# Kernel optimization log

Hardware: AMD Instinct MI355X
Metric: run time of the kernel (lower is better)

## Reference

```python
import jax, jax.numpy as jnp
import numpy as np

B, S, D, H = 4, 2048, 1024, 16
HD = D // H


def setup_inputs() -> dict:
    key = jax.random.key(0)
    ks = jax.random.split(key, 12)
    scale = 1.0 / np.sqrt(D)
    inp = {
        "query": jax.random.normal(ks[0], (B, S, D), jnp.float32),
        "key": jax.random.normal(ks[1], (B, S, D), jnp.float32),
        "value": jax.random.normal(ks[2], (B, S, D), jnp.float32),
        "mask": jax.random.randint(ks[3], (B, 1, S, S), 0, 2).astype(jnp.float32),
        "Wq": jax.random.normal(ks[4], (D, D), jnp.float32) * scale,
        "bq": jnp.zeros((D,), jnp.float32),
        "Wk": jax.random.normal(ks[5], (D, D), jnp.float32) * scale,
        "bk": jnp.zeros((D,), jnp.float32),
        "Wv": jax.random.normal(ks[6], (D, D), jnp.float32) * scale,
        "bv": jnp.zeros((D,), jnp.float32),
        "Wo": jax.random.normal(ks[7], (D, D), jnp.float32) * scale,
        "bo": jnp.zeros((D,), jnp.float32),
    }
    return inp


def reference(query, key, value, mask, Wq, bq, Wk, bk, Wv, bv, Wo, bo):
    # projections, then split heads: [B, S, D] -> [B, H, S, HD]
    def split_heads(x):
        return x.reshape(B, S, H, HD).transpose(0, 2, 1, 3)

    q = split_heads(query @ Wq + bq)
    k = split_heads(key @ Wk + bk)
    v = split_heads(value @ Wv + bv)

    # scores [B, H, Sq, Sk]
    logits = jnp.einsum("bhqd,bhkd->bhqk", q, k) / jnp.sqrt(jnp.float32(HD))
    logits = logits + mask * (-1e9)
    attn = jax.nn.softmax(logits, axis=-1)
    out = jnp.einsum("bhqk,bhkd->bhqd", attn, v)  # [B, H, Sq, HD]
    out = out.transpose(0, 2, 1, 3).reshape(B, S, D)
    return out @ Wo + bo
```

## Files before the change

kernel.cpp:

```cpp
#include <hip/hip_runtime.h>

#define DI __device__ __forceinline__

typedef __attribute__((ext_vector_type(8))) short short8v;
typedef __attribute__((ext_vector_type(4))) float f32x4;

static constexpr int B_ = 4, S_ = 2048, D_ = 1024, H_ = 16, HD_ = 64;
static constexpr int M_ = B_ * S_;

DI unsigned short f2bf(float f) {
  unsigned u = __builtin_bit_cast(unsigned, f);
  u = (u + 0x7fffu + ((u >> 16) & 1u)) >> 16;
  return (unsigned short)u;
}

DI unsigned cvt_pk_bf16(float lo, float hi) {
  unsigned r;
  asm("v_cvt_pk_bf16_f32 %0, %1, %2" : "=v"(r) : "v"(lo), "v"(hi));
  return r;
}

DI void async_copy16(const void* g, void* l) {
  __builtin_amdgcn_global_load_lds((const __attribute__((address_space(1))) void*)g,
                                   (__attribute__((address_space(3))) void*)l, 16, 0, 0);
}

__global__ __launch_bounds__(256) void cast_bf16_kernel(const float* __restrict__ in,
                                                        unsigned short* __restrict__ out,
                                                        int n4) {
  int i = blockIdx.x * blockDim.x + threadIdx.x;
  int stride = gridDim.x * blockDim.x;
  for (; i < n4; i += stride) {
    float4 v = reinterpret_cast<const float4*>(in)[i];
    ushort4 o;
    o.x = f2bf(v.x); o.y = f2bf(v.y); o.z = f2bf(v.z); o.w = f2bf(v.w);
    reinterpret_cast<ushort4*>(out)[i] = o;
  }
}

__global__ __launch_bounds__(256) void transpose_cast_kernel(const float* __restrict__ W,
                                                             unsigned short* __restrict__ Wt,
                                                             int n) {
  __shared__ float t[32][33];
  int bx = blockIdx.x * 32, by = blockIdx.y * 32;
  int x = threadIdx.x, y0 = threadIdx.y;
#pragma unroll
  for (int yy = 0; yy < 32; yy += 8)
    t[y0 + yy][x] = W[(long)(by + y0 + yy) * n + bx + x];
  __syncthreads();
#pragma unroll
  for (int yy = 0; yy < 32; yy += 8)
    Wt[(long)(bx + y0 + yy) * n + by + x] = f2bf(t[x][y0 + yy]);
}

__global__ __launch_bounds__(256) void pack_mask_kernel(const float* __restrict__ mask,
                                                        unsigned long long* __restrict__ bits,
                                                        int nwords) {
  int lane = threadIdx.x & 63;
  int wpb = blockDim.x >> 6;
  int w = blockIdx.x * wpb + (threadIdx.x >> 6);
  int stride = gridDim.x * wpb;
  for (; w < nwords; w += stride) {
    float v = mask[(long)w * 64 + lane];
    unsigned long long b = __ballot(v > 0.5f);
    if (lane == 0) {
      int bb = w >> 16, q = (w >> 5) & 2047, kt64 = w & 31;
      bits[((long)bb << 16) | (kt64 << 11) | q] = b;
    }
  }
}

template <int MODE>
__global__ __launch_bounds__(256) void gemm_bt_kernel(const unsigned short* __restrict__ A,
                                                      const unsigned short* __restrict__ Bt,
                                                      const float* __restrict__ bias,
                                                      void* __restrict__ out,
                                                      int Mdim, int Ndim, int Kdim, float scale) {
  __shared__ unsigned short As[128 * 32];
  __shared__ unsigned short Bs[128 * 32];
  const int tid = threadIdx.x;
  const int lane = tid & 63;
  const int w = tid >> 6;
  const int g = lane >> 4;
  const int l15 = lane & 15;
  const int bm = blockIdx.x * 128;
  const int bn = blockIdx.y * 128;
  const int wr = w >> 1, wc = w & 1;

  f32x4 zero = {0.f, 0.f, 0.f, 0.f};
  f32x4 acc[4][4];
#pragma unroll
  for (int i = 0; i < 4; ++i)
#pragma unroll
    for (int j = 0; j < 4; ++j) acc[i][j] = zero;

  const int srow = lane >> 2;
  const int scol = (lane & 3) * 8;

  for (int k0 = 0; k0 < Kdim; k0 += 32) {
#pragma unroll
    for (int i = 0; i < 2; ++i) {
      int q = w * 2 + i;
      int row = q * 16 + srow;
      async_copy16(&A[(long)(bm + row) * Kdim + k0 + scol], &As[q * 512]);
      async_copy16(&Bt[(long)(bn + row) * Kdim + k0 + scol], &Bs[q * 512]);
    }
    __syncthreads();
    short8v a[4], b[4];
#pragma unroll
    for (int i = 0; i < 4; ++i)
      a[i] = *reinterpret_cast<const short8v*>(&As[(wr * 64 + i * 16 + l15) * 32 + g * 8]);
#pragma unroll
    for (int j = 0; j < 4; ++j)
      b[j] = *reinterpret_cast<const short8v*>(&Bs[(wc * 64 + j * 16 + l15) * 32 + g * 8]);
#pragma unroll
    for (int i = 0; i < 4; ++i)
#pragma unroll
      for (int j = 0; j < 4; ++j)
        acc[i][j] = __builtin_amdgcn_mfma_f32_16x16x32_bf16(a[i], b[j], acc[i][j], 0, 0, 0);
    __syncthreads();
  }

#pragma unroll
  for (int jj = 0; jj < 4; ++jj) {
    int n = bn + wc * 64 + jj * 16 + l15;
    float bs = bias[n];
#pragma unroll
    for (int i = 0; i < 4; ++i) {
      int m0 = bm + wr * 64 + i * 16 + g * 4;
      if (MODE == 0) {
        unsigned short* o = (unsigned short*)out;
#pragma unroll
        for (int r = 0; r < 4; ++r)
          o[(long)(m0 + r) * Ndim + n] = f2bf((acc[i][jj][r] + bs) * scale);
      } else if (MODE == 1) {
        int b2 = m0 >> 11, s0 = m0 & 2047;
        int s0p = (s0 & ~31) | (((s0 >> 2) & 3) << 3) | (((s0 >> 4) & 1) << 2);
        int h2 = n >> 6, d2 = n & 63;
        unsigned short* o = (unsigned short*)out;
        ushort4 v;
        v.x = f2bf(acc[i][jj][0] + bs);
        v.y = f2bf(acc[i][jj][1] + bs);
        v.z = f2bf(acc[i][jj][2] + bs);
        v.w = f2bf(acc[i][jj][3] + bs);
        *reinterpret_cast<ushort4*>(&o[((long)((b2 * 16 + h2) * 64 + d2) << 11) + s0p]) = v;
      } else {
        float* o = (float*)out;
#pragma unroll
        for (int r = 0; r < 4; ++r)
          o[(long)(m0 + r) * Ndim + n] = acc[i][jj][r] + bs;
      }
    }
  }
}

__global__ __launch_bounds__(256, 3) void attn_kernel(const unsigned short* __restrict__ Q,
                                                      const unsigned short* __restrict__ Kb,
                                                      const unsigned short* __restrict__ Vt,
                                                      const unsigned long long* __restrict__ mbits,
                                                      unsigned short* __restrict__ attn) {
  __shared__ unsigned short Ks[64 * 64];
  __shared__ unsigned short Vs[64 * 64];
  const int lane = threadIdx.x & 63;
  const int w = threadIdx.x >> 6;
  const int g = lane >> 4;
  const int l15 = lane & 15;
  const int qt = blockIdx.x;
  const int bh = blockIdx.y;
  const int b = bh >> 4, h = bh & 15;
  const int q0 = qt * 128 + w * 32 + l15;

  const unsigned short* qp = Q + ((long)b * S_ + q0) * D_ + h * HD_ + g * 8;
  short8v qfr[2][2];
  qfr[0][0] = *reinterpret_cast<const short8v*>(qp);
  qfr[0][1] = *reinterpret_cast<const short8v*>(qp + 32);
  qfr[1][0] = *reinterpret_cast<const short8v*>(qp + 16 * D_);
  qfr[1][1] = *reinterpret_cast<const short8v*>(qp + 16 * D_ + 32);

  const int srow = lane >> 3;
  const int schunk = ((lane & 7) ^ (lane >> 3)) * 8;
  const unsigned short* kstage = Kb + (long)b * S_ * D_ + h * HD_;
  const unsigned short* vstage = Vt + (long)bh * HD_ * S_;

  f32x4 zero = {0.f, 0.f, 0.f, 0.f};
  f32x4 oacc[2][4];
#pragma unroll
  for (int qf = 0; qf < 2; ++qf)
#pragma unroll
    for (int d = 0; d < 4; ++d) oacc[qf][d] = zero;
  float m_run[2] = {-1e30f, -1e30f}, l_run[2] = {0.f, 0.f};

  const unsigned long long* mbase = mbits + ((long)b << 16);
  const int swz = l15 & 7;

  for (int kt = 0; kt < S_; kt += 64) {
    unsigned long long mw0 = mbase[((kt >> 6) << 11) + q0];
    unsigned long long mw1 = mbase[((kt >> 6) << 11) + q0 + 16];
#pragma unroll
    for (int i = 0; i < 2; ++i) {
      int blk8 = w * 2 + i;
      async_copy16(&kstage[(long)(kt + blk8 * 8 + srow) * D_ + schunk], &Ks[blk8 * 512]);
      async_copy16(&vstage[(long)(blk8 * 8 + srow) * S_ + kt + schunk], &Vs[blk8 * 512]);
    }
    __syncthreads();

    f32x4 lt[2][4];
#pragma unroll
    for (int g2 = 0; g2 < 4; ++g2) {
      const unsigned short* kr = &Ks[(g2 * 16 + l15) * 64];
      short8v kf0 = *reinterpret_cast<const short8v*>(&kr[(g ^ swz) * 8]);
      short8v kf1 = *reinterpret_cast<const short8v*>(&kr[((g + 4) ^ swz) * 8]);
#pragma unroll
      for (int qf = 0; qf < 2; ++qf) {
        f32x4 c = zero;
        c = __builtin_amdgcn_mfma_f32_16x16x32_bf16(kf0, qfr[qf][0], c, 0, 0, 0);
        c = __builtin_amdgcn_mfma_f32_16x16x32_bf16(kf1, qfr[qf][1], c, 0, 0, 0);
        lt[qf][g2] = c;
      }
    }

    short8v pfr[2][2];
#pragma unroll
    for (int qf = 0; qf < 2; ++qf) {
      unsigned long long mw = qf ? mw1 : mw0;
      float tmax = -1e30f;
#pragma unroll
      for (int g2 = 0; g2 < 4; ++g2)
#pragma unroll
        for (int r = 0; r < 4; ++r) {
          int krel = g2 * 16 + g * 4 + r;
          float v = ((mw >> krel) & 1ull) ? -1e30f : lt[qf][g2][r];
          lt[qf][g2][r] = v;
          tmax = fmaxf(tmax, v);
        }
      tmax = fmaxf(tmax, __shfl_xor(tmax, 16));
      tmax = fmaxf(tmax, __shfl_xor(tmax, 32));
      float m_new = fmaxf(m_run[qf], tmax);
      float alpha = __builtin_amdgcn_exp2f(m_run[qf] - m_new);
      float p[4][4];
      float tsum = 0.f;
#pragma unroll
      for (int g2 = 0; g2 < 4; ++g2)
#pragma unroll
        for (int r = 0; r < 4; ++r) {
          p[g2][r] = __builtin_amdgcn_exp2f(lt[qf][g2][r] - m_new);
          tsum += p[g2][r];
        }
      tsum += __shfl_xor(tsum, 16);
      tsum += __shfl_xor(tsum, 32);
      l_run[qf] = l_run[qf] * alpha + tsum;
      m_run[qf] = m_new;
#pragma unroll
      for (int d = 0; d < 4; ++d) oacc[qf][d] *= alpha;
#pragma unroll
      for (int s = 0; s < 2; ++s) {
        union { unsigned u[4]; short8v v; } pu;
        pu.u[0] = cvt_pk_bf16(p[2 * s][0], p[2 * s][1]);
        pu.u[1] = cvt_pk_bf16(p[2 * s][2], p[2 * s][3]);
        pu.u[2] = cvt_pk_bf16(p[2 * s + 1][0], p[2 * s + 1][1]);
        pu.u[3] = cvt_pk_bf16(p[2 * s + 1][2], p[2 * s + 1][3]);
        pfr[qf][s] = pu.v;
      }
    }

#pragma unroll
    for (int d0 = 0; d0 < 4; ++d0) {
      const unsigned short* vr = &Vs[(d0 * 16 + l15) * 64];
#pragma unroll
      for (int s = 0; s < 2; ++s) {
        short8v vf = *reinterpret_cast<const short8v*>(&vr[((s * 4 + g) ^ swz) * 8]);
#pragma unroll
        for (int qf = 0; qf < 2; ++qf)
          oacc[qf][d0] = __builtin_amdgcn_mfma_f32_16x16x32_bf16(vf, pfr[qf][s], oacc[qf][d0], 0, 0, 0);
      }
    }
    __syncthreads();
  }

#pragma unroll
  for (int qf = 0; qf < 2; ++qf) {
    float inv = 1.f / l_run[qf];
    int q = q0 + qf * 16;
#pragma unroll
    for (int d0 = 0; d0 < 4; ++d0) {
      ushort4 o;
      o.x = f2bf(oacc[qf][d0][0] * inv);
      o.y = f2bf(oacc[qf][d0][1] * inv);
      o.z = f2bf(oacc[qf][d0][2] * inv);
      o.w = f2bf(oacc[qf][d0][3] * inv);
      *reinterpret_cast<ushort4*>(&attn[((long)b * S_ + q) * D_ + h * HD_ + d0 * 16 + g * 4]) = o;
    }
  }
}

extern "C" void kernel_launch(void* const* d_in, const int* in_sizes, int n_in,
                              void* d_out, int out_size, void* d_ws, size_t ws_size,
                              hipStream_t stream) {
  const float* query = (const float*)d_in[0];
  const float* key   = (const float*)d_in[1];
  const float* value = (const float*)d_in[2];
  const float* mask  = (const float*)d_in[3];
  const float* Wq = (const float*)d_in[4];
  const float* bq = (const float*)d_in[5];
  const float* Wk = (const float*)d_in[6];
  const float* bk = (const float*)d_in[7];
  const float* Wv = (const float*)d_in[8];
  const float* bv = (const float*)d_in[9];
  const float* Wo = (const float*)d_in[10];
  const float* bo = (const float*)d_in[11];

  char* ws = (char*)d_ws;
  unsigned short* XQ  = (unsigned short*)(ws);
  unsigned short* XK  = (unsigned short*)(ws + (16ull << 20));
  unsigned short* XV  = (unsigned short*)(ws + (32ull << 20));
  unsigned short* WQT = (unsigned short*)(ws + (48ull << 20));
  unsigned short* WKT = (unsigned short*)(ws + (50ull << 20));
  unsigned short* WVT = (unsigned short*)(ws + (52ull << 20));
  unsigned short* WOT = (unsigned short*)(ws + (54ull << 20));
  unsigned short* QB  = (unsigned short*)(ws + (56ull << 20));
  unsigned short* KB  = (unsigned short*)(ws + (72ull << 20));
  unsigned short* VT  = (unsigned short*)(ws + (88ull << 20));
  unsigned long long* MBITS = (unsigned long long*)(ws + (16ull << 20));
  unsigned short* ATTN = XQ;

  const int n4 = M_ * D_ / 4;
  cast_bf16_kernel<<<2048, 256, 0, stream>>>(query, XQ, n4);
  cast_bf16_kernel<<<2048, 256, 0, stream>>>(key,   XK, n4);
  cast_bf16_kernel<<<2048, 256, 0, stream>>>(value, XV, n4);

  dim3 tg(D_ / 32, D_ / 32), tb(32, 8);
  transpose_cast_kernel<<<tg, tb, 0, stream>>>(Wq, WQT, D_);
  transpose_cast_kernel<<<tg, tb, 0, stream>>>(Wk, WKT, D_);
  transpose_cast_kernel<<<tg, tb, 0, stream>>>(Wv, WVT, D_);
  transpose_cast_kernel<<<tg, tb, 0, stream>>>(Wo, WOT, D_);

  dim3 gg(M_ / 128, D_ / 128);
  gemm_bt_kernel<0><<<gg, 256, 0, stream>>>(XQ, WQT, bq, QB, M_, D_, D_, 0.18033688011112042f);
  gemm_bt_kernel<0><<<gg, 256, 0, stream>>>(XK, WKT, bk, KB, M_, D_, D_, 1.f);
  gemm_bt_kernel<1><<<gg, 256, 0, stream>>>(XV, WVT, bv, VT, M_, D_, D_, 1.f);

  pack_mask_kernel<<<2048, 256, 0, stream>>>(mask, MBITS, B_ * S_ * S_ / 64);

  dim3 ag(S_ / 128, B_ * H_);
  attn_kernel<<<ag, 256, 0, stream>>>(QB, KB, VT, MBITS, ATTN);

  gemm_bt_kernel<2><<<gg, 256, 0, stream>>>(ATTN, WOT, bo, d_out, M_, D_, D_, 1.f);
}
```

Measured before the change: 311.2 us.

## Double-buffer K/V tiles in attention with async prefetch of next tile

New measurement: 318.0 us. 1.02x slower.

```diff
diff --git a/kernel.cpp b/kernel.cpp
--- a/kernel.cpp
+++ b/kernel.cpp
@@ -154,13 +154,13 @@
   }
 }
 
-__global__ __launch_bounds__(256, 3) void attn_kernel(const unsigned short* __restrict__ Q,
+__global__ __launch_bounds__(256, 2) void attn_kernel(const unsigned short* __restrict__ Q,
                                                       const unsigned short* __restrict__ Kb,
                                                       const unsigned short* __restrict__ Vt,
                                                       const unsigned long long* __restrict__ mbits,
                                                       unsigned short* __restrict__ attn) {
-  __shared__ unsigned short Ks[64 * 64];
-  __shared__ unsigned short Vs[64 * 64];
+  __shared__ unsigned short Ks[2][64 * 64];
+  __shared__ unsigned short Vs[2][64 * 64];
   const int lane = threadIdx.x & 63;
   const int w = threadIdx.x >> 6;
   const int g = lane >> 4;
@@ -193,21 +193,41 @@
   const unsigned long long* mbase = mbits + ((long)b << 16);
   const int swz = l15 & 7;
 
-  for (int kt = 0; kt < S_; kt += 64) {
-    unsigned long long mw0 = mbase[((kt >> 6) << 11) + q0];
-    unsigned long long mw1 = mbase[((kt >> 6) << 11) + q0 + 16];
+  auto stage = [&](int kt, int bi) {
 #pragma unroll
     for (int i = 0; i < 2; ++i) {
       int blk8 = w * 2 + i;
-      async_copy16(&kstage[(long)(kt + blk8 * 8 + srow) * D_ + schunk], &Ks[blk8 * 512]);
-      async_copy16(&vstage[(long)(blk8 * 8 + srow) * S_ + kt + schunk], &Vs[blk8 * 512]);
-    }
-    __syncthreads();
+      async_copy16(&kstage[(long)(kt + blk8 * 8 + srow) * D_ + schunk], &Ks[bi][blk8 * 512]);
+      async_copy16(&vstage[(long)(blk8 * 8 + srow) * S_ + kt + schunk], &Vs[bi][blk8 * 512]);
+    }
+  };
+
+  unsigned long long mw_cur0 = mbase[q0];
+  unsigned long long mw_cur1 = mbase[q0 + 16];
+  stage(0, 0);
+
+  int cur = 0;
+  for (int t = 0; t < S_ / 64; ++t) {
+    const int kt = t * 64;
+    unsigned long long mw_nxt0 = 0, mw_nxt1 = 0;
+    if (t < S_ / 64 - 1) {
+      mw_nxt0 = mbase[(((t + 1)) << 11) + q0];
+      mw_nxt1 = mbase[(((t + 1)) << 11) + q0 + 16];
+      stage(kt + 64, cur ^ 1);
+      asm volatile("s_waitcnt vmcnt(6)" ::: "memory");
+    } else {
+      asm volatile("s_waitcnt vmcnt(0)" ::: "memory");
+    }
+    __builtin_amdgcn_s_barrier();
+    asm volatile("" ::: "memory");
+
+    const unsigned short* Kbuf = &Ks[cur][0];
+    const unsigned short* Vbuf = &Vs[cur][0];
 
     f32x4 lt[2][4];
 #pragma unroll
     for (int g2 = 0; g2 < 4; ++g2) {
-      const unsigned short* kr = &Ks[(g2 * 16 + l15) * 64];
+      const unsigned short* kr = &Kbuf[(g2 * 16 + l15) * 64];
       short8v kf0 = *reinterpret_cast<const short8v*>(&kr[(g ^ swz) * 8]);
       short8v kf1 = *reinterpret_cast<const short8v*>(&kr[((g + 4) ^ swz) * 8]);
 #pragma unroll
@@ -222,7 +242,7 @@
     short8v pfr[2][2];
 #pragma unroll
     for (int qf = 0; qf < 2; ++qf) {
-      unsigned long long mw = qf ? mw1 : mw0;
+      unsigned long long mw = qf ? mw_cur1 : mw_cur0;
       float tmax = -1e30f;
 #pragma unroll
       for (int g2 = 0; g2 < 4; ++g2)
@@ -265,7 +285,7 @@
 
 #pragma unroll
     for (int d0 = 0; d0 < 4; ++d0) {
-      const unsigned short* vr = &Vs[(d0 * 16 + l15) * 64];
+      const unsigned short* vr = &Vbuf[(d0 * 16 + l15) * 64];
 #pragma unroll
       for (int s = 0; s < 2; ++s) {
         short8v vf = *reinterpret_cast<const short8v*>(&vr[((s * 4 + g) ^ swz) * 8]);
@@ -274,7 +294,13 @@
           oacc[qf][d0] = __builtin_amdgcn_mfma_f32_16x16x32_bf16(vf, pfr[qf][s], oacc[qf][d0], 0, 0, 0);
       }
     }
-    __syncthreads();
+
+    asm volatile("" ::: "memory");
+    __builtin_amdgcn_s_barrier();
+    asm volatile("" ::: "memory");
+    mw_cur0 = mw_nxt0;
+    mw_cur1 = mw_nxt1;
+    cur ^= 1;
   }
 
 #pragma unroll
```
